# Kernel tuning notes

Measured on AMD Instinct MI355X. Metric: run time of the kernel, lower is better.

Reference implementation:

```python
import jax, jax.numpy as jnp
import numpy as np

N = 100000
E = 1200000
D = 64  # in_dim == out_dim


def leaky_relu(x, slope=0.2):
    return jnp.where(x >= 0, x, slope * x)


def setup_inputs() -> dict:
    key = jax.random.key(0)
    ks = jax.random.split(key, 10)
    indices = jax.random.randint(ks[0], (2, E), 0, N, dtype=jnp.int64)
    features = jax.random.normal(ks[1], (N, D), dtype=jnp.float32)
    e_r = jax.random.normal(ks[2], (E, D), dtype=jnp.float32)
    s = 1.0 / np.sqrt(D)
    W1_w = jax.random.normal(ks[3], (D, D), dtype=jnp.float32) * s
    W1_b = jax.random.normal(ks[4], (D,), dtype=jnp.float32) * s
    W2_w = jax.random.normal(ks[5], (D, D), dtype=jnp.float32) * s
    W2_b = jax.random.normal(ks[6], (D,), dtype=jnp.float32) * s
    Watt_w = jax.random.normal(ks[7], (D, D), dtype=jnp.float32) * s
    Watt_b = jax.random.normal(ks[8], (D,), dtype=jnp.float32) * s
    return {"indices": indices, "features": features, "e_r": e_r, "num_nodes": N,
            "W1_w": W1_w, "W1_b": W1_b, "W2_w": W2_w, "W2_b": W2_b,
            "Watt_w": Watt_w, "Watt_b": Watt_b}


def reference(indices, features, e_r, num_nodes, W1_w, W1_b, W2_w, W2_b, Watt_w, Watt_b):
    src, dst = indices[0], indices[1]
    out_dim = Watt_w.shape[0]

    # edge attention scores
    h_trans = features @ Watt_w.T + Watt_b          # (N, D)
    h_src = h_trans[src]                            # (E, D) gather
    h_dst = h_trans[dst]                            # (E, D) gather
    # e_r already aligned to out_dim (d_r == out_dim here)
    e_raw = jnp.sum(h_dst * jnp.tanh(h_src + e_r), axis=-1, keepdims=True)  # (E, 1)
    scaling = 1.0 / (out_dim ** 0.5)
    e_ij = leaky_relu(e_raw * scaling).astype(jnp.float32)

    # segment softmax over edges grouped by dst (max detached, as in original)
    max_score = jax.ops.segment_max(jax.lax.stop_gradient(e_ij), dst,
                                    num_segments=num_nodes)               # (N, 1)
    exp_e = jnp.exp(e_ij - max_score[dst])                                 # (E, 1)
    denom = jax.ops.segment_sum(exp_e, dst, num_segments=num_nodes)       # (N, 1)
    alpha = exp_e / (denom[dst] + 1e-9)                                    # (E, 1)

    # weighted scatter aggregation
    weighted_msg = features[src] * alpha.astype(features.dtype)            # (E, D)
    h_neigh = jax.ops.segment_sum(weighted_msg, dst, num_segments=num_nodes)  # (N, D)

    sum_h = features + h_neigh
    prod_h = features * h_neigh
    h_out = leaky_relu(sum_h @ W1_w.T + W1_b + (prod_h @ W2_w.T + W2_b))
    return h_out
```

## Files before the change

kernel.cpp:

```cpp
#include <hip/hip_runtime.h>
#include <hip/hip_bf16.h>

#define D 64
#define SCAN_CHUNK 2048

__device__ __forceinline__ float fast_tanh(float x) {
    float e2 = __expf(2.0f * x);
    return 1.0f - 2.0f / (e2 + 1.0f);
}

__device__ __forceinline__ float leaky(float x) {
    return x >= 0.0f ? x : 0.2f * x;
}

__global__ __launch_bounds__(256) void k_htrans(const float* __restrict__ feat,
                                                const float* __restrict__ W,
                                                const float* __restrict__ bias,
                                                float* __restrict__ out, int N)
{
    __shared__ float Wt[D][D];
    __shared__ float bsh[D];
    __shared__ float fs[32][D + 1];
    const int t = threadIdx.x;
    for (int i = t; i < D * D; i += 256) { Wt[i & 63][i >> 6] = W[i]; }
    if (t < D) bsh[t] = bias[t];
    const int cg = t & 15;
    const int rp = t >> 4;
    for (int g = 0; g < 2; ++g) {
        const int base = blockIdx.x * 64 + g * 32;
        __syncthreads();
        for (int i = t; i < 32 * D; i += 256) {
            int r = i >> 6, d = i & 63;
            int n = base + r;
            fs[r][d] = (n < N) ? feat[(size_t)n * D + d] : 0.0f;
        }
        __syncthreads();
        float4 acc0 = {0, 0, 0, 0}, acc1 = {0, 0, 0, 0};
        const int r0 = rp * 2, r1 = r0 + 1;
        #pragma unroll 8
        for (int d = 0; d < D; ++d) {
            const float4 w = *reinterpret_cast<const float4*>(&Wt[d][cg * 4]);
            const float f0 = fs[r0][d], f1 = fs[r1][d];
            acc0.x += f0 * w.x; acc0.y += f0 * w.y; acc0.z += f0 * w.z; acc0.w += f0 * w.w;
            acc1.x += f1 * w.x; acc1.y += f1 * w.y; acc1.z += f1 * w.z; acc1.w += f1 * w.w;
        }
        const float4 b4 = *reinterpret_cast<const float4*>(&bsh[cg * 4]);
        const int n0 = base + r0, n1 = base + r1;
        if (n0 < N) {
            float4 o = {acc0.x + b4.x, acc0.y + b4.y, acc0.z + b4.z, acc0.w + b4.w};
            *reinterpret_cast<float4*>(&out[(size_t)n0 * D + cg * 4]) = o;
        }
        if (n1 < N) {
            float4 o = {acc1.x + b4.x, acc1.y + b4.y, acc1.z + b4.z, acc1.w + b4.w};
            *reinterpret_cast<float4*>(&out[(size_t)n1 * D + cg * 4]) = o;
        }
    }
}

__global__ __launch_bounds__(256) void k_hist(const int* __restrict__ dst, int* __restrict__ cnt, int E)
{
    int e = blockIdx.x * 256 + threadIdx.x;
    if (e < E) atomicAdd(&cnt[dst[e]], 1);
}

__global__ __launch_bounds__(256) void k_scan1(int* __restrict__ offs, int* __restrict__ partials, int N)
{
    __shared__ int lds[256];
    const int t = threadIdx.x;
    const int base = blockIdx.x * SCAN_CHUNK + t * 8;
    int v[8];
    #pragma unroll
    for (int i = 0; i < 8; ++i) v[i] = (base + i < N) ? offs[base + i] : 0;
    int tot = 0;
    #pragma unroll
    for (int i = 0; i < 8; ++i) { int x = v[i]; v[i] = tot; tot += x; }
    lds[t] = tot;
    __syncthreads();
    for (int off = 1; off < 256; off <<= 1) {
        int x = 0;
        if (t >= off) x = lds[t - off];
        __syncthreads();
        lds[t] += x;
        __syncthreads();
    }
    const int texc = (t == 0) ? 0 : lds[t - 1];
    #pragma unroll
    for (int i = 0; i < 8; ++i)
        if (base + i < N) offs[base + i] = v[i] + texc;
    if (t == 255) partials[blockIdx.x] = lds[255];
}

__global__ void k_scan2(int* __restrict__ partials, int NB)
{
    if (threadIdx.x == 0 && blockIdx.x == 0) {
        int run = 0;
        for (int i = 0; i < NB; ++i) { int x = partials[i]; partials[i] = run; run += x; }
    }
}

__global__ __launch_bounds__(256) void k_scan3(int* __restrict__ offs, const int* __restrict__ partials, int N)
{
    const int add = partials[blockIdx.x];
    if (add == 0) return;
    const int base = blockIdx.x * SCAN_CHUNK + threadIdx.x * 8;
    #pragma unroll
    for (int i = 0; i < 8; ++i)
        if (base + i < N) offs[base + i] += add;
}

__global__ __launch_bounds__(256) void k_scatter(const int* __restrict__ dst, int* __restrict__ offs,
                                                 int* __restrict__ eid, int E)
{
    int e = blockIdx.x * 256 + threadIdx.x;
    if (e < E) {
        int pos = atomicAdd(&offs[dst[e]], 1);
        eid[pos] = e;
    }
}

__global__ __launch_bounds__(256) void k_fused(const int* __restrict__ src,
                                               const int* __restrict__ eid,
                                               const int* __restrict__ offs,
                                               const float* __restrict__ ht,
                                               const float* __restrict__ er,
                                               const float* __restrict__ feat,
                                               float* __restrict__ hneigh, int N)
{
    const int t = threadIdx.x;
    const int lane = t & 15;
    const int n = blockIdx.x * 16 + (t >> 4);
    if (n >= N) return;
    const int beg = (n == 0) ? 0 : offs[n - 1];
    const int end = offs[n];
    const float4 hd = *reinterpret_cast<const float4*>(ht + (size_t)n * D + lane * 4);
    float4 acc = {0, 0, 0, 0};
    float den = 0.0f;
    for (int p = beg; p < end; ++p) {
        const int e = eid[p];
        const int s = src[e];
        const float4 hs = *reinterpret_cast<const float4*>(ht + (size_t)s * D + lane * 4);
        const float4 ev = *reinterpret_cast<const float4*>(er + (size_t)e * D + lane * 4);
        const float4 f  = *reinterpret_cast<const float4*>(feat + (size_t)s * D + lane * 4);
        float pp = hd.x * fast_tanh(hs.x + ev.x)
                 + hd.y * fast_tanh(hs.y + ev.y)
                 + hd.z * fast_tanh(hs.z + ev.z)
                 + hd.w * fast_tanh(hs.w + ev.w);
        pp += __shfl_xor(pp, 1);
        pp += __shfl_xor(pp, 2);
        pp += __shfl_xor(pp, 4);
        pp += __shfl_xor(pp, 8);
        const float ex = __expf(leaky(pp * 0.125f));
        den += ex;
        acc.x += ex * f.x; acc.y += ex * f.y; acc.z += ex * f.z; acc.w += ex * f.w;
    }
    const float r = __builtin_amdgcn_rcpf(den + 1e-9f);
    float4 o = {acc.x * r, acc.y * r, acc.z * r, acc.w * r};
    *reinterpret_cast<float4*>(hneigh + (size_t)n * D + lane * 4) = o;
}

__global__ __launch_bounds__(256) void k_out(const float* __restrict__ feat,
                                             const float* __restrict__ hneigh,
                                             const float* __restrict__ W1,
                                             const float* __restrict__ b1,
                                             const float* __restrict__ W2,
                                             const float* __restrict__ b2,
                                             float* __restrict__ out, int N)
{
    __shared__ float W1t[D][D];
    __shared__ float W2t[D][D];
    __shared__ float bsum[D];
    __shared__ float ss[32][D + 1];
    __shared__ float pp[32][D + 1];
    const int t = threadIdx.x;
    for (int i = t; i < D * D; i += 256) {
        W1t[i & 63][i >> 6] = W1[i];
        W2t[i & 63][i >> 6] = W2[i];
    }
    if (t < D) bsum[t] = b1[t] + b2[t];
    const int cg = t & 15;
    const int rp = t >> 4;
    for (int g = 0; g < 2; ++g) {
        const int base = blockIdx.x * 64 + g * 32;
        __syncthreads();
        for (int i = t; i < 32 * D; i += 256) {
            int r = i >> 6, d = i & 63;
            int n = base + r;
            float f = 0.0f, hn = 0.0f;
            if (n < N) { f = feat[(size_t)n * D + d]; hn = hneigh[(size_t)n * D + d]; }
            ss[r][d] = f + hn;
            pp[r][d] = f * hn;
        }
        __syncthreads();
        float4 a0 = {0, 0, 0, 0}, a1 = {0, 0, 0, 0};
        const int r0 = rp * 2, r1 = r0 + 1;
        #pragma unroll 4
        for (int d = 0; d < D; ++d) {
            const float4 w1 = *reinterpret_cast<const float4*>(&W1t[d][cg * 4]);
            const float4 w2 = *reinterpret_cast<const float4*>(&W2t[d][cg * 4]);
            const float s0 = ss[r0][d], p0 = pp[r0][d];
            const float s1 = ss[r1][d], p1 = pp[r1][d];
            a0.x += s0 * w1.x + p0 * w2.x; a0.y += s0 * w1.y + p0 * w2.y;
            a0.z += s0 * w1.z + p0 * w2.z; a0.w += s0 * w1.w + p0 * w2.w;
            a1.x += s1 * w1.x + p1 * w2.x; a1.y += s1 * w1.y + p1 * w2.y;
            a1.z += s1 * w1.z + p1 * w2.z; a1.w += s1 * w1.w + p1 * w2.w;
        }
        const float4 b4 = *reinterpret_cast<const float4*>(&bsum[cg * 4]);
        const int n0 = base + r0, n1 = base + r1;
        if (n0 < N) {
            float4 o = {leaky(a0.x + b4.x), leaky(a0.y + b4.y), leaky(a0.z + b4.z), leaky(a0.w + b4.w)};
            *reinterpret_cast<float4*>(&out[(size_t)n0 * D + cg * 4]) = o;
        }
        if (n1 < N) {
            float4 o = {leaky(a1.x + b4.x), leaky(a1.y + b4.y), leaky(a1.z + b4.z), leaky(a1.w + b4.w)};
            *reinterpret_cast<float4*>(&out[(size_t)n1 * D + cg * 4]) = o;
        }
    }
}

extern "C" void kernel_launch(void* const* d_in, const int* in_sizes, int n_in,
                              void* d_out, int out_size, void* d_ws, size_t ws_size,
                              hipStream_t stream) {
    const int*   idx  = (const int*)d_in[0];
    const float* feat = (const float*)d_in[1];
    const float* er   = (const float*)d_in[2];
    const float* W1   = (const float*)d_in[4];
    const float* b1   = (const float*)d_in[5];
    const float* W2   = (const float*)d_in[6];
    const float* b2   = (const float*)d_in[7];
    const float* Wa   = (const float*)d_in[8];
    const float* ba   = (const float*)d_in[9];

    const int E = in_sizes[0] / 2;
    const int N = in_sizes[1] / D;
    const int* srcI = idx;
    const int* dstI = idx + E;

    float* htrans = (float*)d_out;
    float* hneigh   = (float*)d_ws;
    int*   offs     = (int*)(hneigh + (size_t)N * D);
    int*   partials = offs + N;
    int*   eid      = partials + 256;

    const int NB = (N + SCAN_CHUNK - 1) / SCAN_CHUNK;

    hipMemsetAsync(offs, 0, (size_t)N * sizeof(int), stream);

    dim3 blk(256);
    k_htrans <<<dim3((N + 63) / 64), blk, 0, stream>>>(feat, Wa, ba, htrans, N);
    k_hist   <<<dim3((E + 255) / 256), blk, 0, stream>>>(dstI, offs, E);
    k_scan1  <<<dim3(NB), blk, 0, stream>>>(offs, partials, N);
    k_scan2  <<<dim3(1), dim3(64), 0, stream>>>(partials, NB);
    k_scan3  <<<dim3(NB), blk, 0, stream>>>(offs, partials, N);
    k_scatter<<<dim3((E + 255) / 256), blk, 0, stream>>>(dstI, offs, eid, E);
    k_fused  <<<dim3((N + 15) / 16), blk, 0, stream>>>(srcI, eid, offs, htrans, er, feat, hneigh, N);
    k_out    <<<dim3((N + 63) / 64), blk, 0, stream>>>(feat, hneigh, W1, b1, W2, b2, (float*)d_out, N);
}
```

Before: 767.0 us.

## Split each node's edges across four subgroups and pack edge/src pairs

The fused aggregation kernel now gives each destination node a full 64-lane wavefront. Four 16-lane subgroups process interleaved edges, and their partial sums are combined at the end with cross-lane shuffles. The scatter step stores (edge id, src) pairs, which removes the dependent src[e] lookup, and the next pair is prefetched one iteration ahead. This raises memory-level parallelism for low-degree nodes, at the cost of idle lanes when a node has fewer than four edges and a larger workspace for the pair array.

```diff
diff --git a/kernel.cpp b/kernel.cpp
--- a/kernel.cpp
+++ b/kernel.cpp
@@ -108,18 +108,19 @@
         if (base + i < N) offs[base + i] += add;
 }
 
-__global__ __launch_bounds__(256) void k_scatter(const int* __restrict__ dst, int* __restrict__ offs,
-                                                 int* __restrict__ eid, int E)
+__global__ __launch_bounds__(256) void k_scatter(const int* __restrict__ dst,
+                                                 const int* __restrict__ srcA,
+                                                 int* __restrict__ offs,
+                                                 int2* __restrict__ es, int E)
 {
     int e = blockIdx.x * 256 + threadIdx.x;
     if (e < E) {
         int pos = atomicAdd(&offs[dst[e]], 1);
-        eid[pos] = e;
-    }
-}
-
-__global__ __launch_bounds__(256) void k_fused(const int* __restrict__ src,
-                                               const int* __restrict__ eid,
+        es[pos] = make_int2(e, srcA[e]);
+    }
+}
+
+__global__ __launch_bounds__(256) void k_fused(const int2* __restrict__ es,
                                                const int* __restrict__ offs,
                                                const float* __restrict__ ht,
                                                const float* __restrict__ er,
@@ -127,20 +128,26 @@
                                                float* __restrict__ hneigh, int N)
 {
     const int t = threadIdx.x;
-    const int lane = t & 15;
-    const int n = blockIdx.x * 16 + (t >> 4);
+    const int lane = t & 63;
+    const int n = blockIdx.x * 4 + (t >> 6);
     if (n >= N) return;
+    const int sg = lane >> 4;
+    const int dl = lane & 15;
     const int beg = (n == 0) ? 0 : offs[n - 1];
     const int end = offs[n];
-    const float4 hd = *reinterpret_cast<const float4*>(ht + (size_t)n * D + lane * 4);
+    const float4 hd = *reinterpret_cast<const float4*>(ht + (size_t)n * D + dl * 4);
     float4 acc = {0, 0, 0, 0};
     float den = 0.0f;
-    for (int p = beg; p < end; ++p) {
-        const int e = eid[p];
-        const int s = src[e];
-        const float4 hs = *reinterpret_cast<const float4*>(ht + (size_t)s * D + lane * 4);
-        const float4 ev = *reinterpret_cast<const float4*>(er + (size_t)e * D + lane * 4);
-        const float4 f  = *reinterpret_cast<const float4*>(feat + (size_t)s * D + lane * 4);
+    int p = beg + sg;
+    int2 cur = make_int2(0, 0);
+    if (p < end) cur = es[p];
+    while (p < end) {
+        const int pn = p + 4;
+        int2 nxt = make_int2(0, 0);
+        if (pn < end) nxt = es[pn];
+        const float4 ev = *reinterpret_cast<const float4*>(er + (size_t)cur.x * D + dl * 4);
+        const float4 hs = *reinterpret_cast<const float4*>(ht + (size_t)cur.y * D + dl * 4);
+        const float4 f  = *reinterpret_cast<const float4*>(feat + (size_t)cur.y * D + dl * 4);
         float pp = hd.x * fast_tanh(hs.x + ev.x)
                  + hd.y * fast_tanh(hs.y + ev.y)
                  + hd.z * fast_tanh(hs.z + ev.z)
@@ -152,10 +159,20 @@
         const float ex = __expf(leaky(pp * 0.125f));
         den += ex;
         acc.x += ex * f.x; acc.y += ex * f.y; acc.z += ex * f.z; acc.w += ex * f.w;
-    }
-    const float r = __builtin_amdgcn_rcpf(den + 1e-9f);
-    float4 o = {acc.x * r, acc.y * r, acc.z * r, acc.w * r};
-    *reinterpret_cast<float4*>(hneigh + (size_t)n * D + lane * 4) = o;
+        cur = nxt;
+        p = pn;
+    }
+    den += __shfl_xor(den, 16);
+    den += __shfl_xor(den, 32);
+    acc.x += __shfl_xor(acc.x, 16); acc.x += __shfl_xor(acc.x, 32);
+    acc.y += __shfl_xor(acc.y, 16); acc.y += __shfl_xor(acc.y, 32);
+    acc.z += __shfl_xor(acc.z, 16); acc.z += __shfl_xor(acc.z, 32);
+    acc.w += __shfl_xor(acc.w, 16); acc.w += __shfl_xor(acc.w, 32);
+    if (sg == 0) {
+        const float r = __builtin_amdgcn_rcpf(den + 1e-9f);
+        float4 o = {acc.x * r, acc.y * r, acc.z * r, acc.w * r};
+        *reinterpret_cast<float4*>(hneigh + (size_t)n * D + dl * 4) = o;
+    }
 }
 
 __global__ __launch_bounds__(256) void k_out(const float* __restrict__ feat,
@@ -239,7 +256,7 @@
     float* hneigh   = (float*)d_ws;
     int*   offs     = (int*)(hneigh + (size_t)N * D);
     int*   partials = offs + N;
-    int*   eid      = partials + 256;
+    int2*  es       = (int2*)(partials + 256);
 
     const int NB = (N + SCAN_CHUNK - 1) / SCAN_CHUNK;
 
@@ -251,7 +268,7 @@
     k_scan1  <<<dim3(NB), blk, 0, stream>>>(offs, partials, N);
     k_scan2  <<<dim3(1), dim3(64), 0, stream>>>(partials, NB);
     k_scan3  <<<dim3(NB), blk, 0, stream>>>(offs, partials, N);
-    k_scatter<<<dim3((E + 255) / 256), blk, 0, stream>>>(dstI, offs, eid, E);
-    k_fused  <<<dim3((N + 15) / 16), blk, 0, stream>>>(srcI, eid, offs, htrans, er, feat, hneigh, N);
+    k_scatter<<<dim3((E + 255) / 256), blk, 0, stream>>>(dstI, srcI, offs, es, E);
+    k_fused  <<<dim3((N + 3) / 4), blk, 0, stream>>>(es, offs, htrans, er, feat, hneigh, N);
     k_out    <<<dim3((N + 63) / 64), blk, 0, stream>>>(feat, hneigh, W1, b1, W2, b2, (float*)d_out, N);
 }
```

New measurement: 729.9 us. 4.8% less time.
